# Optimization experiments

Hardware: AMD Instinct MI355X
Metric: run time of the kernel (lower is better)

The kernel has to match this reference:

```python
import jax, jax.numpy as jnp
import numpy as np

DIM = 192
NUM_HEADS = 6
KERNELS = [3, 5, 7]
DILATIONS = [1, 2, 3]
NBRANCH = 3
HEADS_B = NUM_HEADS // NBRANCH      # heads per branch = 2
HEAD_DIM = DIM // NUM_HEADS         # 32


def _axis_idx(L, K, d):
    """NATTEN-style neighborhood indices along one axis with dilation.
    Returns (nbr[L,K] absolute neighbor positions, bias[L,K] rpb indices in [0, 2K-2]).
    """
    i = np.arange(L)
    g = i % d                                 # dilation group
    ii = i // d                               # index within subgrid
    Lg = (L - g + d - 1) // d                 # subgrid length of each group
    start = np.clip(ii - K // 2, 0, Lg - K)   # clamp window inside bounds
    ki = np.arange(K)
    nbr = g[:, None] + (start[:, None] + ki[None, :]) * d        # [L,K]
    bias = start[:, None] + ki[None, :] - ii[:, None] + (K - 1)  # [L,K]
    return nbr, bias


def _branch(xb, K, d, rpb):
    # xb: [B,H,W, 3*heads*head_dim] laid out as (3, heads, head_dim)
    B, H, W, _ = xb.shape
    qkv = xb.reshape(B, H, W, 3, HEADS_B, HEAD_DIM).transpose(3, 0, 4, 1, 2, 5)
    q, k, v = qkv[0], qkv[1], qkv[2]          # [B,h,H,W,hd]
    q = q * (HEAD_DIM ** -0.5)
    nh, bh = _axis_idx(H, K, d)
    nw, bw = _axis_idx(W, K, d)
    # gather K x K neighborhoods: [B,h,H,W,K,K,hd]
    k_nb = k[:, :, nh[:, None, :, None], nw[None, :, None, :]]
    attn = jnp.einsum('bhijd,bhijkld->bhijkl', q, k_nb)
    attn = attn + rpb[:, bh[:, None, :, None], bw[None, :, None, :]][None]
    attn = jax.nn.softmax(attn.reshape(B, HEADS_B, H, W, K * K), axis=-1)
    attn = attn.reshape(B, HEADS_B, H, W, K, K)
    v_nb = v[:, :, nh[:, None, :, None], nw[None, :, None, :]]
    y = jnp.einsum('bhijkl,bhijkld->bhijd', attn, v_nb)
    return y.transpose(0, 2, 3, 1, 4).reshape(B, H, W, HEADS_B * HEAD_DIM)


def setup_inputs() -> dict:
    key = jax.random.key(0)
    ks = jax.random.split(key, 8)
    B, H, W = 8, 64, 64
    return {
        'x': jax.random.normal(ks[0], (B, DIM, H, W), jnp.float32),
        'qkv_w': jax.random.normal(ks[1], (3 * DIM, DIM), jnp.float32) * 0.02,
        'qkv_b': jnp.zeros((3 * DIM,), jnp.float32),
        'proj_w': jax.random.normal(ks[2], (DIM, DIM), jnp.float32) * 0.02,
        'proj_b': jnp.zeros((DIM,), jnp.float32),
        'rpb0': jax.random.normal(ks[3], (HEADS_B, 5, 5), jnp.float32) * 0.02,
        'rpb1': jax.random.normal(ks[4], (HEADS_B, 9, 9), jnp.float32) * 0.02,
        'rpb2': jax.random.normal(ks[5], (HEADS_B, 13, 13), jnp.float32) * 0.02,
    }


def reference(x, qkv_w, qkv_b, proj_w, proj_b, rpb0, rpb1, rpb2):
    # x: [B,C,H,W] -> BHWC
    xp = x.transpose(0, 2, 3, 1)
    qkv = xp @ qkv_w.T + qkv_b                 # [B,H,W,3*dim]
    branches = jnp.split(qkv, NBRANCH, axis=-1)  # equal channels (dim divisible by k)
    rpbs = [rpb0, rpb1, rpb2]
    ys = [_branch(branches[i], KERNELS[i], DILATIONS[i], rpbs[i]) for i in range(NBRANCH)]
    out = jnp.concatenate(ys, axis=-1) @ proj_w.T + proj_b
    return out.transpose(0, 3, 1, 2)
```

## Files before the change

kernel.cpp:

```cpp
#include <hip/hip_runtime.h>
#include <stdint.h>

typedef __attribute__((ext_vector_type(4))) float f32x4;
typedef _Float16 half8 __attribute__((ext_vector_type(8)));
typedef _Float16 half2v __attribute__((ext_vector_type(2)));

#define LDK 200
#define QSCALE 0.17677669529663689f

__device__ __forceinline__ float dot2f(unsigned int k2, unsigned int q2, float c) {
#if __has_builtin(__builtin_amdgcn_fdot2)
  return __builtin_amdgcn_fdot2(__builtin_bit_cast(half2v, k2),
                                __builtin_bit_cast(half2v, q2), c, false);
#else
  half2v a = __builtin_bit_cast(half2v, k2), b = __builtin_bit_cast(half2v, q2);
  return c + (float)a.x * (float)b.x + (float)a.y * (float)b.y;
#endif
}

__global__ __launch_bounds__(256) void prep_w(
    const float* __restrict__ qw, const float* __restrict__ qb,
    const float* __restrict__ pw,
    _Float16* __restrict__ qwh, float* __restrict__ qbs, _Float16* __restrict__ pwh) {
  int i = blockIdx.x * 256 + threadIdx.x;
  if (i < 27648) {
    float4 v = ((const float4*)qw)[i];
    int n = (i * 4) / 192;
    float sc = ((n % 192) < 64) ? QSCALE : 1.0f;
    _Float16* d = qwh + i * 4;
    d[0] = (_Float16)(v.x * sc); d[1] = (_Float16)(v.y * sc);
    d[2] = (_Float16)(v.z * sc); d[3] = (_Float16)(v.w * sc);
  } else if (i < 36864) {
    int k = i - 27648;
    float4 v = ((const float4*)pw)[k];
    _Float16* d = pwh + k * 4;
    d[0] = (_Float16)v.x; d[1] = (_Float16)v.y;
    d[2] = (_Float16)v.z; d[3] = (_Float16)v.w;
  } else if (i < 36864 + 576) {
    int n = i - 36864;
    qbs[n] = qb[n] * (((n % 192) < 64) ? QSCALE : 1.0f);
  }
}

__global__ __launch_bounds__(256) void qkv_gemm(
    const float* __restrict__ x, const _Float16* __restrict__ wh,
    const float* __restrict__ qbs, _Float16* __restrict__ qkv) {
  __shared__ _Float16 Al[64 * LDK];
  const int t = threadIdx.x;
  const int tm = blockIdx.x;
  const int ng = blockIdx.y;
  const int bb = (tm * 64) >> 12, hw0 = (tm * 64) & 4095;
  const float* xb = x + (size_t)bb * 192 * 4096 + hw0;

  #pragma unroll
  for (int j = 0; j < 12; ++j) {
    int idx = j * 256 + t;
    int m4 = (idx & 15) * 4, c = idx >> 4;
    float4 v = *(const float4*)(xb + (size_t)c * 4096 + m4);
    Al[(m4 + 0) * LDK + c] = (_Float16)v.x;
    Al[(m4 + 1) * LDK + c] = (_Float16)v.y;
    Al[(m4 + 2) * LDK + c] = (_Float16)v.z;
    Al[(m4 + 3) * LDK + c] = (_Float16)v.w;
  }
  __syncthreads();

  const int lane = t & 63, wid = t >> 6;
  const int wm = (wid >> 1) * 32, wn = (wid & 1) * 32;
  const int lr = lane & 15, kb = (lane >> 4) * 8;
  const int r0 = (lane >> 4) * 4;
  _Float16* opb = qkv + (size_t)(tm * 64) * 576;

  for (int n0 = ng * 192; n0 < ng * 192 + 192; n0 += 64) {
    f32x4 acc[2][2];
    #pragma unroll
    for (int i = 0; i < 2; ++i)
      #pragma unroll
      for (int j = 0; j < 2; ++j)
        #pragma unroll
        for (int r = 0; r < 4; ++r) acc[i][j][r] = 0.0f;

    #pragma unroll
    for (int kk = 0; kk < 192; kk += 32) {
      half8 a0 = *(const half8*)&Al[(wm + lr) * LDK + kk + kb];
      half8 a1 = *(const half8*)&Al[(wm + 16 + lr) * LDK + kk + kb];
      half8 b0 = *(const half8*)(wh + (size_t)(n0 + wn + lr) * 192 + kk + kb);
      half8 b1 = *(const half8*)(wh + (size_t)(n0 + wn + 16 + lr) * 192 + kk + kb);
      acc[0][0] = __builtin_amdgcn_mfma_f32_16x16x32_f16(a0, b0, acc[0][0], 0, 0, 0);
      acc[0][1] = __builtin_amdgcn_mfma_f32_16x16x32_f16(a0, b1, acc[0][1], 0, 0, 0);
      acc[1][0] = __builtin_amdgcn_mfma_f32_16x16x32_f16(a1, b0, acc[1][0], 0, 0, 0);
      acc[1][1] = __builtin_amdgcn_mfma_f32_16x16x32_f16(a1, b1, acc[1][1], 0, 0, 0);
    }

    #pragma unroll
    for (int i = 0; i < 2; ++i)
      #pragma unroll
      for (int j = 0; j < 2; ++j) {
        int gn = n0 + wn + j * 16 + lr;
        float bs = qbs[gn];
        #pragma unroll
        for (int r = 0; r < 4; ++r) {
          int row = wm + i * 16 + r0 + r;
          opb[row * 576 + gn] = (_Float16)(acc[i][j][r] + bs);
        }
      }
  }
}

template <int K, int DIL>
__device__ __forceinline__ void natten_branch(
    const _Float16* __restrict__ qkv, const float* __restrict__ rpb,
    _Float16* __restrict__ yo, const int branch, const int r,
    unsigned short* __restrict__ smem) {
  constexpr int RW = 2 * K - 1;
  constexpr int H8 = K + 7;
  constexpr int NH = H8 * H8;
  constexpr int NL = (K * K + 3) / 4;
  constexpr int LSTR = 40;

  _Float16* Kl = (_Float16*)smem;
  _Float16* Vl = Kl + NH * LSTR;
  _Float16* Ql = Vl + NH * LSTR;
  float* rs = (float*)(Ql + 64 * LSTR);

  const int t = threadIdx.x;
  const int bh = r & 15;
  const int head = bh & 1, bb = bh >> 1;
  const int rr = r >> 4;
  int gh, gw, ti, tj, Lgh, Lgw;
  if (DIL == 1) {
    gh = 0; gw = 0; ti = (rr >> 3) * 8; tj = (rr & 7) * 8; Lgh = 64; Lgw = 64;
  } else if (DIL == 2) {
    int cls = rr >> 4, tile = rr & 15;
    gh = cls >> 1; gw = cls & 1; ti = (tile >> 2) * 8; tj = (tile & 3) * 8;
    Lgh = 32; Lgw = 32;
  } else {
    int cls = rr / 9, tile = rr % 9;
    gh = cls / 3; gw = cls % 3; ti = (tile / 3) * 8; tj = (tile % 3) * 8;
    Lgh = (64 - gh + 2) / 3; Lgw = (64 - gw + 2) / 3;
  }
  const int hoh = max(0, min(ti - K / 2, Lgh - K));
  const int how = max(0, min(tj - K / 2, Lgw - K));

  for (int i = t; i < RW * RW; i += 256) rs[i] = rpb[head * RW * RW + i];

  const _Float16* kvb = qkv + (size_t)bb * 4096 * 576 + branch * 192 + 64 + head * 32;
  for (int L = t; L < NH * 8; L += 256) {
    int px = L >> 3, part = L & 7;
    int hr = px / H8, hc = px % H8;
    int cr = min(hoh + hr, Lgh - 1), cc = min(how + hc, Lgw - 1);
    int ph = gh + cr * DIL, pw2 = gw + cc * DIL;
    const _Float16* src = kvb + (size_t)(ph * 64 + pw2) * 576 + (part & 3) * 8 + ((part & 4) ? 64 : 0);
    _Float16* dst = ((part & 4) ? Vl : Kl) + px * LSTR + (part & 3) * 8;
    *(uint4*)dst = *(const uint4*)src;
  }
  {
    int qi = t >> 2, part = t & 3;
    int ci0 = min(ti + (qi >> 3), Lgh - 1), cj0 = min(tj + (qi & 7), Lgw - 1);
    int ph = gh + ci0 * DIL, pw2 = gw + cj0 * DIL;
    const _Float16* src = qkv + (size_t)((size_t)bb * 4096 + ph * 64 + pw2) * 576
                          + branch * 192 + head * 32 + part * 8;
    *(uint4*)(Ql + qi * LSTR + part * 8) = *(const uint4*)src;
  }
  __syncthreads();

  const int qi = t >> 2, sl = t & 3;
  const int ci = ti + (qi >> 3), cj = tj + (qi & 7);
  const bool valid = (ci < Lgh) && (cj < Lgw);

  int s0h = ci - K / 2; if (s0h < 0) s0h = 0; if (s0h > Lgh - K) s0h = Lgh - K;
  int s0w = cj - K / 2; if (s0w < 0) s0w = 0; if (s0w > Lgw - K) s0w = Lgw - K;
  const int rbase = s0h - hoh, cbase = s0w - how;
  const int bhb = s0h - ci + K - 1, bwb = s0w - cj + K - 1;

  unsigned int qh[16];
  #pragma unroll
  for (int u = 0; u < 4; ++u) {
    uint4 v = *(const uint4*)(Ql + qi * LSTR + u * 8);
    qh[u * 4 + 0] = v.x; qh[u * 4 + 1] = v.y; qh[u * 4 + 2] = v.z; qh[u * 4 + 3] = v.w;
  }

  float s[NL];
  float mx = -1e30f;
  #pragma unroll
  for (int j = 0; j < NL; ++j) {
    int n = sl + 4 * j;
    if (n < K * K) {
      int kh = n / K, kw = n % K;
      int lidx = (rbase + kh) * H8 + (cbase + kw);
      const _Float16* kp = Kl + lidx * LSTR;
      float sc = rs[(bhb + kh) * RW + (bwb + kw)];
      #pragma unroll
      for (int u = 0; u < 4; ++u) {
        uint4 kv = *(const uint4*)(kp + u * 8);
        sc = dot2f(kv.x, qh[4 * u + 0], sc);
        sc = dot2f(kv.y, qh[4 * u + 1], sc);
        sc = dot2f(kv.z, qh[4 * u + 2], sc);
        sc = dot2f(kv.w, qh[4 * u + 3], sc);
      }
      s[j] = sc;
      mx = fmaxf(mx, sc);
    } else {
      s[j] = -1e30f;
    }
  }
  mx = fmaxf(mx, __shfl_xor(mx, 1, 64));
  mx = fmaxf(mx, __shfl_xor(mx, 2, 64));

  float pw[NL];
  float l = 0.0f;
  #pragma unroll
  for (int j = 0; j < NL; ++j) { pw[j] = __expf(s[j] - mx); l += pw[j]; }
  l += __shfl_xor(l, 1, 64);
  l += __shfl_xor(l, 2, 64);

  half2v acch[16];
  #pragma unroll
  for (int i = 0; i < 16; ++i) acch[i] = (half2v)(_Float16)0.0f;
  #pragma unroll
  for (int j = 0; j < NL; ++j) {
    int n = sl + 4 * j;
    if (n < K * K) {
      int kh = n / K, kw = n % K;
      int lidx = (rbase + kh) * H8 + (cbase + kw);
      const _Float16* vp = Vl + lidx * LSTR;
      _Float16 ph = (_Float16)pw[j];
      half2v pp = {ph, ph};
      #pragma unroll
      for (int u = 0; u < 4; ++u) {
        uint4 vv = *(const uint4*)(vp + u * 8);
        acch[4 * u + 0] += pp * __builtin_bit_cast(half2v, vv.x);
        acch[4 * u + 1] += pp * __builtin_bit_cast(half2v, vv.y);
        acch[4 * u + 2] += pp * __builtin_bit_cast(half2v, vv.z);
        acch[4 * u + 3] += pp * __builtin_bit_cast(half2v, vv.w);
      }
    }
  }
  #pragma unroll
  for (int st = 1; st <= 2; st <<= 1) {
    #pragma unroll
    for (int i = 0; i < 16; ++i) {
      unsigned int o = __shfl_xor(__builtin_bit_cast(unsigned int, acch[i]), st, 64);
      acch[i] += __builtin_bit_cast(half2v, o);
    }
  }

  if (valid) {
    float inv = 1.0f / l;
    _Float16 ih = (_Float16)inv;
    half2v iv = {ih, ih};
    unsigned int a[16];
    #pragma unroll
    for (int i = 0; i < 16; ++i) a[i] = __builtin_bit_cast(unsigned int, acch[i]);
    uint4 pk;
    unsigned int r0, r1, r2, r3;
    r0 = (sl < 2) ? ((sl == 0) ? a[0] : a[4]) : ((sl == 2) ? a[8] : a[12]);
    r1 = (sl < 2) ? ((sl == 0) ? a[1] : a[5]) : ((sl == 2) ? a[9] : a[13]);
    r2 = (sl < 2) ? ((sl == 0) ? a[2] : a[6]) : ((sl == 2) ? a[10] : a[14]);
    r3 = (sl < 2) ? ((sl == 0) ? a[3] : a[7]) : ((sl == 2) ? a[11] : a[15]);
    pk.x = __builtin_bit_cast(unsigned int, __builtin_bit_cast(half2v, r0) * iv);
    pk.y = __builtin_bit_cast(unsigned int, __builtin_bit_cast(half2v, r1) * iv);
    pk.z = __builtin_bit_cast(unsigned int, __builtin_bit_cast(half2v, r2) * iv);
    pk.w = __builtin_bit_cast(unsigned int, __builtin_bit_cast(half2v, r3) * iv);
    const int p = bb * 4096 + (gh + ci * DIL) * 64 + (gw + cj * DIL);
    *(uint4*)(yo + (size_t)p * 192 + branch * 64 + head * 32 + sl * 8) = pk;
  }
}

__global__ __launch_bounds__(256) void natten_all(
    const _Float16* __restrict__ qkv,
    const float* __restrict__ rpb0, const float* __restrict__ rpb1,
    const float* __restrict__ rpb2, _Float16* __restrict__ yo) {
  __shared__ __align__(16) unsigned short smem[18624];
  const int gid = blockIdx.x;
  if (gid < 1296)       natten_branch<7, 3>(qkv, rpb2, yo, 2, gid, smem);
  else if (gid < 2320)  natten_branch<5, 2>(qkv, rpb1, yo, 1, gid - 1296, smem);
  else                  natten_branch<3, 1>(qkv, rpb0, yo, 0, gid - 2320, smem);
}

__global__ __launch_bounds__(256) void proj_gemm(
    const _Float16* __restrict__ y, const _Float16* __restrict__ wh,
    const float* __restrict__ bias, float* __restrict__ out) {
  __shared__ _Float16 Bl[64 * LDK];
  const int t = threadIdx.x;
  const int tp = blockIdx.x;
  const int c0 = blockIdx.y * 64;

  const _Float16* ybp = y + (size_t)(tp * 64) * 192;
  #pragma unroll
  for (int j = 0; j < 6; ++j) {
    int idx = j * 256 + t;
    int m = idx / 24, k8 = (idx % 24) * 8;
    *(uint4*)&Bl[m * LDK + k8] = *(const uint4*)(ybp + m * 192 + k8);
  }
  __syncthreads();

  const int lane = t & 63, wid = t >> 6;
  const int wm = (wid >> 1) * 32, wn = (wid & 1) * 32;
  const int lr = lane & 15, kb = (lane >> 4) * 8;
  const int r0 = (lane >> 4) * 4;
  const int gp = tp * 64;
  const int bb = gp >> 12, hw0 = gp & 4095;
  float* op = out + (size_t)bb * 192 * 4096 + hw0;

  f32x4 acc[2][2];
  #pragma unroll
  for (int i = 0; i < 2; ++i)
    #pragma unroll
    for (int j = 0; j < 2; ++j)
      #pragma unroll
      for (int r = 0; r < 4; ++r) acc[i][j][r] = 0.0f;

  #pragma unroll
  for (int kk = 0; kk < 192; kk += 32) {
    half8 a0 = *(const half8*)(wh + (size_t)(c0 + wm + lr) * 192 + kk + kb);
    half8 a1 = *(const half8*)(wh + (size_t)(c0 + wm + 16 + lr) * 192 + kk + kb);
    half8 b0 = *(const half8*)&Bl[(wn + lr) * LDK + kk + kb];
    half8 b1 = *(const half8*)&Bl[(wn + 16 + lr) * LDK + kk + kb];
    acc[0][0] = __builtin_amdgcn_mfma_f32_16x16x32_f16(a0, b0, acc[0][0], 0, 0, 0);
    acc[0][1] = __builtin_amdgcn_mfma_f32_16x16x32_f16(a0, b1, acc[0][1], 0, 0, 0);
    acc[1][0] = __builtin_amdgcn_mfma_f32_16x16x32_f16(a1, b0, acc[1][0], 0, 0, 0);
    acc[1][1] = __builtin_amdgcn_mfma_f32_16x16x32_f16(a1, b1, acc[1][1], 0, 0, 0);
  }

  #pragma unroll
  for (int i = 0; i < 2; ++i)
    #pragma unroll
    for (int j = 0; j < 2; ++j) {
      int m = wn + j * 16 + lr;
      #pragma unroll
      for (int r = 0; r < 4; ++r) {
        int c = c0 + wm + i * 16 + r0 + r;
        op[(size_t)c * 4096 + m] = acc[i][j][r] + bias[c];
      }
    }
}

extern "C" void kernel_launch(void* const* d_in, const int* in_sizes, int n_in,
                              void* d_out, int out_size, void* d_ws, size_t ws_size,
                              hipStream_t stream) {
  const float* x      = (const float*)d_in[0];
  const float* qkv_w  = (const float*)d_in[1];
  const float* qkv_b  = (const float*)d_in[2];
  const float* proj_w = (const float*)d_in[3];
  const float* proj_b = (const float*)d_in[4];
  const float* rpb0   = (const float*)d_in[5];
  const float* rpb1   = (const float*)d_in[6];
  const float* rpb2   = (const float*)d_in[7];

  _Float16* qkv = (_Float16*)d_ws;
  _Float16* yb  = qkv + (size_t)32768 * 576;
  _Float16* qwh = yb + (size_t)32768 * 192;
  float*    qbs = (float*)(qwh + 110592);
  _Float16* pwh = (_Float16*)(qbs + 576);
  float* out = (float*)d_out;

  prep_w<<<dim3(147), 256, 0, stream>>>(qkv_w, qkv_b, proj_w, qwh, qbs, pwh);
  qkv_gemm<<<dim3(512, 3), 256, 0, stream>>>(x, qwh, qbs, qkv);
  natten_all<<<dim3(3344), 256, 0, stream>>>(qkv, rpb0, rpb1, rpb2, yb);
  proj_gemm<<<dim3(512, 3), 256, 0, stream>>>(yb, pwh, proj_b, out);
}
```

Measured before the change: 161.0 us.

## Pre-transpose x to fp16, register-cache weights, double-buffer tiles in GEMMs

Moves the NCHW-to-NHWC fp16 conversion of x into the prep kernel, writing an fp16 copy to workspace. The QKV GEMM then holds its weight slice in registers and loops over four 64-pixel tiles, prefetching the next tile into registers while computing the current one. The projection GEMM does the same over two pixel tiles. The aim is to stop re-reading and re-converting fp32 x once per output group, and to hide load latency behind MFMA work, at the cost of an extra fp16 round trip of x through global memory and more registers.

```diff
diff --git a/kernel.cpp b/kernel.cpp
--- a/kernel.cpp
+++ b/kernel.cpp
@@ -18,59 +18,89 @@
 #endif
 }
 
-__global__ __launch_bounds__(256) void prep_w(
-    const float* __restrict__ qw, const float* __restrict__ qb,
-    const float* __restrict__ pw,
-    _Float16* __restrict__ qwh, float* __restrict__ qbs, _Float16* __restrict__ pwh) {
-  int i = blockIdx.x * 256 + threadIdx.x;
-  if (i < 27648) {
-    float4 v = ((const float4*)qw)[i];
-    int n = (i * 4) / 192;
-    float sc = ((n % 192) < 64) ? QSCALE : 1.0f;
-    _Float16* d = qwh + i * 4;
-    d[0] = (_Float16)(v.x * sc); d[1] = (_Float16)(v.y * sc);
-    d[2] = (_Float16)(v.z * sc); d[3] = (_Float16)(v.w * sc);
-  } else if (i < 36864) {
-    int k = i - 27648;
-    float4 v = ((const float4*)pw)[k];
-    _Float16* d = pwh + k * 4;
-    d[0] = (_Float16)v.x; d[1] = (_Float16)v.y;
-    d[2] = (_Float16)v.z; d[3] = (_Float16)v.w;
-  } else if (i < 36864 + 576) {
-    int n = i - 36864;
-    qbs[n] = qb[n] * (((n % 192) < 64) ? QSCALE : 1.0f);
+#define MFMA16(A, B, C) __builtin_amdgcn_mfma_f32_16x16x32_f16(A, B, C, 0, 0, 0)
+
+__global__ __launch_bounds__(256) void prep(
+    const float* __restrict__ x, const float* __restrict__ qw,
+    const float* __restrict__ qb, const float* __restrict__ pw,
+    _Float16* __restrict__ xh, _Float16* __restrict__ qwh,
+    float* __restrict__ qbs, _Float16* __restrict__ pwh) {
+  __shared__ _Float16 T[64 * LDK];
+  const int bx = blockIdx.x, t = threadIdx.x;
+  if (bx < 512) {
+    const int bb = bx >> 6, hw0 = (bx & 63) << 6;
+    const float* xb = x + (size_t)bb * 192 * 4096 + hw0;
+    #pragma unroll
+    for (int j = 0; j < 12; ++j) {
+      int idx = j * 256 + t;
+      int m4 = (idx & 15) * 4, c = idx >> 4;
+      float4 v = *(const float4*)(xb + (size_t)c * 4096 + m4);
+      T[(m4 + 0) * LDK + c] = (_Float16)v.x;
+      T[(m4 + 1) * LDK + c] = (_Float16)v.y;
+      T[(m4 + 2) * LDK + c] = (_Float16)v.z;
+      T[(m4 + 3) * LDK + c] = (_Float16)v.w;
+    }
+    __syncthreads();
+    _Float16* xo = xh + ((size_t)bb * 4096 + hw0) * 192;
+    #pragma unroll
+    for (int j = 0; j < 6; ++j) {
+      int idx = j * 256 + t;
+      int m = idx / 24, k8 = (idx % 24) * 8;
+      *(uint4*)(xo + m * 192 + k8) = *(const uint4*)&T[m * LDK + k8];
+    }
+  } else {
+    int i = (bx - 512) * 256 + t;
+    if (i < 27648) {
+      float4 v = ((const float4*)qw)[i];
+      int n = (i * 4) / 192;
+      float sc = ((n % 192) < 64) ? QSCALE : 1.0f;
+      _Float16* d = qwh + i * 4;
+      d[0] = (_Float16)(v.x * sc); d[1] = (_Float16)(v.y * sc);
+      d[2] = (_Float16)(v.z * sc); d[3] = (_Float16)(v.w * sc);
+    } else if (i < 36864) {
+      int k = i - 27648;
+      float4 v = ((const float4*)pw)[k];
+      _Float16* d = pwh + k * 4;
+      d[0] = (_Float16)v.x; d[1] = (_Float16)v.y;
+      d[2] = (_Float16)v.z; d[3] = (_Float16)v.w;
+    } else if (i < 36864 + 576) {
+      int n = i - 36864;
+      qbs[n] = qb[n] * (((n % 192) < 64) ? QSCALE : 1.0f);
+    }
   }
 }
 
 __global__ __launch_bounds__(256) void qkv_gemm(
-    const float* __restrict__ x, const _Float16* __restrict__ wh,
+    const _Float16* __restrict__ xh, const _Float16* __restrict__ wh,
     const float* __restrict__ qbs, _Float16* __restrict__ qkv) {
   __shared__ _Float16 Al[64 * LDK];
   const int t = threadIdx.x;
-  const int tm = blockIdx.x;
-  const int ng = blockIdx.y;
-  const int bb = (tm * 64) >> 12, hw0 = (tm * 64) & 4095;
-  const float* xb = x + (size_t)bb * 192 * 4096 + hw0;
-
-  #pragma unroll
-  for (int j = 0; j < 12; ++j) {
-    int idx = j * 256 + t;
-    int m4 = (idx & 15) * 4, c = idx >> 4;
-    float4 v = *(const float4*)(xb + (size_t)c * 4096 + m4);
-    Al[(m4 + 0) * LDK + c] = (_Float16)v.x;
-    Al[(m4 + 1) * LDK + c] = (_Float16)v.y;
-    Al[(m4 + 2) * LDK + c] = (_Float16)v.z;
-    Al[(m4 + 3) * LDK + c] = (_Float16)v.w;
-  }
-  __syncthreads();
-
+  const int n0 = blockIdx.y << 6;
+  const int p0 = blockIdx.x << 8;
   const int lane = t & 63, wid = t >> 6;
   const int wm = (wid >> 1) * 32, wn = (wid & 1) * 32;
   const int lr = lane & 15, kb = (lane >> 4) * 8;
   const int r0 = (lane >> 4) * 4;
-  _Float16* opb = qkv + (size_t)(tm * 64) * 576;
-
-  for (int n0 = ng * 192; n0 < ng * 192 + 192; n0 += 64) {
+
+  half8 B0[6], B1[6];
+  #pragma unroll
+  for (int k6 = 0; k6 < 6; ++k6) {
+    B0[k6] = *(const half8*)(wh + (size_t)(n0 + wn + lr) * 192 + k6 * 32 + kb);
+    B1[k6] = *(const half8*)(wh + (size_t)(n0 + wn + 16 + lr) * 192 + k6 * 32 + kb);
+  }
+  const float bs0 = qbs[n0 + wn + lr], bs1 = qbs[n0 + wn + 16 + lr];
+
+  uint4 pf[6];
+#define QSTAGE_LOAD(TT) { const _Float16* src = xh + ((size_t)p0 + (TT) * 64) * 192; \
+  _Pragma("unroll") for (int q = 0; q < 6; ++q) pf[q] = *(const uint4*)(src + (q * 256 + t) * 8); }
+#define QSTAGE_WRITE() { _Pragma("unroll") for (int q = 0; q < 6; ++q) { int id = q * 256 + t; \
+  *(uint4*)&Al[(id / 24) * LDK + (id % 24) * 8] = pf[q]; } }
+
+  QSTAGE_LOAD(0); QSTAGE_WRITE(); __syncthreads();
+
+  for (int tt = 0; tt < 4; ++tt) {
+    if (tt < 3) QSTAGE_LOAD(tt + 1);
+
     f32x4 acc[2][2];
     #pragma unroll
     for (int i = 0; i < 2; ++i)
@@ -80,30 +110,32 @@
         for (int r = 0; r < 4; ++r) acc[i][j][r] = 0.0f;
 
     #pragma unroll
-    for (int kk = 0; kk < 192; kk += 32) {
-      half8 a0 = *(const half8*)&Al[(wm + lr) * LDK + kk + kb];
-      half8 a1 = *(const half8*)&Al[(wm + 16 + lr) * LDK + kk + kb];
-      half8 b0 = *(const half8*)(wh + (size_t)(n0 + wn + lr) * 192 + kk + kb);
-      half8 b1 = *(const half8*)(wh + (size_t)(n0 + wn + 16 + lr) * 192 + kk + kb);
-      acc[0][0] = __builtin_amdgcn_mfma_f32_16x16x32_f16(a0, b0, acc[0][0], 0, 0, 0);
-      acc[0][1] = __builtin_amdgcn_mfma_f32_16x16x32_f16(a0, b1, acc[0][1], 0, 0, 0);
-      acc[1][0] = __builtin_amdgcn_mfma_f32_16x16x32_f16(a1, b0, acc[1][0], 0, 0, 0);
-      acc[1][1] = __builtin_amdgcn_mfma_f32_16x16x32_f16(a1, b1, acc[1][1], 0, 0, 0);
-    }
-
+    for (int k6 = 0; k6 < 6; ++k6) {
+      half8 a0 = *(const half8*)&Al[(wm + lr) * LDK + k6 * 32 + kb];
+      half8 a1 = *(const half8*)&Al[(wm + 16 + lr) * LDK + k6 * 32 + kb];
+      acc[0][0] = MFMA16(a0, B0[k6], acc[0][0]);
+      acc[0][1] = MFMA16(a0, B1[k6], acc[0][1]);
+      acc[1][0] = MFMA16(a1, B0[k6], acc[1][0]);
+      acc[1][1] = MFMA16(a1, B1[k6], acc[1][1]);
+    }
+
+    _Float16* opb = qkv + ((size_t)p0 + tt * 64) * 576 + n0;
     #pragma unroll
     for (int i = 0; i < 2; ++i)
       #pragma unroll
       for (int j = 0; j < 2; ++j) {
-        int gn = n0 + wn + j * 16 + lr;
-        float bs = qbs[gn];
+        int col = wn + j * 16 + lr;
+        float bs = j ? bs1 : bs0;
         #pragma unroll
-        for (int r = 0; r < 4; ++r) {
-          int row = wm + i * 16 + r0 + r;
-          opb[row * 576 + gn] = (_Float16)(acc[i][j][r] + bs);
-        }
+        for (int r = 0; r < 4; ++r)
+          opb[(wm + i * 16 + r0 + r) * 576 + col] = (_Float16)(acc[i][j][r] + bs);
       }
-  }
+
+    __syncthreads();
+    if (tt < 3) { QSTAGE_WRITE(); __syncthreads(); }
+  }
+#undef QSTAGE_LOAD
+#undef QSTAGE_WRITE
 }
 
 template <int K, int DIL>
@@ -282,57 +314,74 @@
     const float* __restrict__ bias, float* __restrict__ out) {
   __shared__ _Float16 Bl[64 * LDK];
   const int t = threadIdx.x;
-  const int tp = blockIdx.x;
-  const int c0 = blockIdx.y * 64;
-
-  const _Float16* ybp = y + (size_t)(tp * 64) * 192;
-  #pragma unroll
-  for (int j = 0; j < 6; ++j) {
-    int idx = j * 256 + t;
-    int m = idx / 24, k8 = (idx % 24) * 8;
-    *(uint4*)&Bl[m * LDK + k8] = *(const uint4*)(ybp + m * 192 + k8);
-  }
-  __syncthreads();
-
+  const int c0 = blockIdx.y << 6;
+  const int p0 = blockIdx.x << 7;
   const int lane = t & 63, wid = t >> 6;
   const int wm = (wid >> 1) * 32, wn = (wid & 1) * 32;
   const int lr = lane & 15, kb = (lane >> 4) * 8;
   const int r0 = (lane >> 4) * 4;
-  const int gp = tp * 64;
-  const int bb = gp >> 12, hw0 = gp & 4095;
-  float* op = out + (size_t)bb * 192 * 4096 + hw0;
-
-  f32x4 acc[2][2];
+
+  half8 A0[6], A1[6];
+  #pragma unroll
+  for (int k6 = 0; k6 < 6; ++k6) {
+    A0[k6] = *(const half8*)(wh + (size_t)(c0 + wm + lr) * 192 + k6 * 32 + kb);
+    A1[k6] = *(const half8*)(wh + (size_t)(c0 + wm + 16 + lr) * 192 + k6 * 32 + kb);
+  }
+  float bi[2][4];
   #pragma unroll
   for (int i = 0; i < 2; ++i)
     #pragma unroll
-    for (int j = 0; j < 2; ++j)
-      #pragma unroll
-      for (int r = 0; r < 4; ++r) acc[i][j][r] = 0.0f;
-
-  #pragma unroll
-  for (int kk = 0; kk < 192; kk += 32) {
-    half8 a0 = *(const half8*)(wh + (size_t)(c0 + wm + lr) * 192 + kk + kb);
-    half8 a1 = *(const half8*)(wh + (size_t)(c0 + wm + 16 + lr) * 192 + kk + kb);
-    half8 b0 = *(const half8*)&Bl[(wn + lr) * LDK + kk + kb];
-    half8 b1 = *(const half8*)&Bl[(wn + 16 + lr) * LDK + kk + kb];
-    acc[0][0] = __builtin_amdgcn_mfma_f32_16x16x32_f16(a0, b0, acc[0][0], 0, 0, 0);
-    acc[0][1] = __builtin_amdgcn_mfma_f32_16x16x32_f16(a0, b1, acc[0][1], 0, 0, 0);
-    acc[1][0] = __builtin_amdgcn_mfma_f32_16x16x32_f16(a1, b0, acc[1][0], 0, 0, 0);
-    acc[1][1] = __builtin_amdgcn_mfma_f32_16x16x32_f16(a1, b1, acc[1][1], 0, 0, 0);
-  }
-
-  #pragma unroll
-  for (int i = 0; i < 2; ++i)
-    #pragma unroll
-    for (int j = 0; j < 2; ++j) {
-      int m = wn + j * 16 + lr;
-      #pragma unroll
-      for (int r = 0; r < 4; ++r) {
-        int c = c0 + wm + i * 16 + r0 + r;
-        op[(size_t)c * 4096 + m] = acc[i][j][r] + bias[c];
+    for (int r = 0; r < 4; ++r) bi[i][r] = bias[c0 + wm + i * 16 + r0 + r];
+
+  uint4 pf[6];
+#define PSTAGE_LOAD(TT) { const _Float16* src = y + ((size_t)p0 + (TT) * 64) * 192; \
+  _Pragma("unroll") for (int q = 0; q < 6; ++q) pf[q] = *(const uint4*)(src + (q * 256 + t) * 8); }
+#define PSTAGE_WRITE() { _Pragma("unroll") for (int q = 0; q < 6; ++q) { int id = q * 256 + t; \
+  *(uint4*)&Bl[(id / 24) * LDK + (id % 24) * 8] = pf[q]; } }
+
+  PSTAGE_LOAD(0); PSTAGE_WRITE(); __syncthreads();
+
+  for (int tt = 0; tt < 2; ++tt) {
+    if (tt < 1) PSTAGE_LOAD(tt + 1);
+
+    f32x4 acc[2][2];
+    #pragma unroll
+    for (int i = 0; i < 2; ++i)
+      #pragma unroll
+      for (int j = 0; j < 2; ++j)
+        #pragma unroll
+        for (int r = 0; r < 4; ++r) acc[i][j][r] = 0.0f;
+
+    #pragma unroll
+    for (int k6 = 0; k6 < 6; ++k6) {
+      half8 b0 = *(const half8*)&Bl[(wn + lr) * LDK + k6 * 32 + kb];
+      half8 b1 = *(const half8*)&Bl[(wn + 16 + lr) * LDK + k6 * 32 + kb];
+      acc[0][0] = MFMA16(A0[k6], b0, acc[0][0]);
+      acc[0][1] = MFMA16(A0[k6], b1, acc[0][1]);
+      acc[1][0] = MFMA16(A1[k6], b0, acc[1][0]);
+      acc[1][1] = MFMA16(A1[k6], b1, acc[1][1]);
+    }
+
+    const int gp = p0 + tt * 64;
+    const int bb = gp >> 12, hw0 = gp & 4095;
+    float* op = out + (size_t)bb * 192 * 4096 + hw0;
+    #pragma unroll
+    for (int i = 0; i < 2; ++i)
+      #pragma unroll
+      for (int j = 0; j < 2; ++j) {
+        int m = wn + j * 16 + lr;
+        #pragma unroll
+        for (int r = 0; r < 4; ++r) {
+          int c = c0 + wm + i * 16 + r0 + r;
+          op[(size_t)c * 4096 + m] = acc[i][j][r] + bi[i][r];
+        }
       }
-    }
+
+    __syncthreads();
+    if (tt < 1) { PSTAGE_WRITE(); __syncthreads(); }
+  }
+#undef PSTAGE_LOAD
+#undef PSTAGE_WRITE
 }
 
 extern "C" void kernel_launch(void* const* d_in, const int* in_sizes, int n_in,
@@ -349,13 +398,14 @@
 
   _Float16* qkv = (_Float16*)d_ws;
   _Float16* yb  = qkv + (size_t)32768 * 576;
-  _Float16* qwh = yb + (size_t)32768 * 192;
-  float*    qbs = (float*)(qwh + 110592);
-  _Float16* pwh = (_Float16*)(qbs + 576);
+  _Float16* xh  = yb + (size_t)32768 * 192;
+  _Float16* qwh = xh + (size_t)32768 * 192;
+  _Float16* pwh = qwh + 110592;
+  float*    qbs = (float*)(pwh + 36864);
   float* out = (float*)d_out;
 
-  prep_w<<<dim3(147), 256, 0, stream>>>(qkv_w, qkv_b, proj_w, qwh, qbs, pwh);
-  qkv_gemm<<<dim3(512, 3), 256, 0, stream>>>(x, qwh, qbs, qkv);
+  prep<<<dim3(659), 256, 0, stream>>>(x, qkv_w, qkv_b, proj_w, xh, qwh, qbs, pwh);
+  qkv_gemm<<<dim3(128, 9), 256, 0, stream>>>(xh, qwh, qbs, qkv);
   natten_all<<<dim3(3344), 256, 0, stream>>>(qkv, rpb0, rpb1, rpb2, yb);
-  proj_gemm<<<dim3(512, 3), 256, 0, stream>>>(yb, pwh, proj_b, out);
-}
+  proj_gemm<<<dim3(256, 3), 256, 0, stream>>>(yb, pwh, proj_b, out);
+}
```

Result: slower. 176.6 us (+9.7%).
